# Optimization experiments

Measured on AMD Instinct MI355X. Metric: run time of the kernel, lower is better.

## Reference

```python
import jax, jax.numpy as jnp
import numpy as np

N_ATOMS = 32768
N_EDGES = 262144
ATOM_F = 256
EDGE_F = 128
OUT_F = 512
N_GAUSS = 50
SPIN_D = 3


def setup_inputs() -> dict:
    key = jax.random.key(0)
    k1, k2, k3, k4, k5 = jax.random.split(key, 5)
    h = jax.random.normal(k1, (N_ATOMS, ATOM_F), dtype=jnp.float32)
    m = jax.random.normal(k2, (N_EDGES, EDGE_F), dtype=jnp.float32)
    magft_cat = jax.random.normal(k3, (N_ATOMS, SPIN_D), dtype=jnp.float32)
    edge_index = jax.random.randint(k4, (2, N_EDGES), 0, N_ATOMS, dtype=jnp.int64)
    in_f = 2 * ATOM_F + EDGE_F + N_GAUSS  # 690
    W = jax.random.normal(k5, (OUT_F, in_f), dtype=jnp.float32) * 0.02
    return {"h": h, "m": m, "magft_cat": magft_cat, "edge_index": edge_index, "W": W}


def reference(h, m, magft_cat, edge_index, W):
    # GaussianSmearing(-1.5, 1.5, 50)
    offsets = jnp.linspace(-1.5, 1.5, N_GAUSS, dtype=jnp.float32)  # (G,)
    coeff = -0.5 / (offsets[1] - offsets[0]) ** 2

    src = edge_index[0]
    tgt = edge_index[1]
    h_s = h[src]                     # (E, A)
    h_t = h[tgt]                     # (E, A)
    # per-edge spin dot product, (E, 1)
    d = jnp.sum(magft_cat[src] * magft_cat[tgt], axis=1, keepdims=True)
    spin_edge = jnp.exp(coeff * (d - offsets) ** 2)  # (E, G)
    m_st = jnp.concatenate([h_s, h_t, m, spin_edge], axis=-1)  # (E, 690)
    # bias-free Dense with activation=None
    return m_st @ W.T  # (E, OUT_F)
```

## Files before the change

kernel.cpp:

```cpp
#include <hip/hip_runtime.h>
#include <hip/hip_bf16.h>

#define N_ATOMS 32768
#define N_EDGESC 262144
#define ATOM_F 256
#define EDGE_F 128
#define OUT_F 512
#define N_GAUSS 50
#define IN_F 690
#define NCHUNK 11

#define BM 128
#define BN 256
#define NTHREADS 512

using f32x4  = __attribute__((ext_vector_type(4))) float;
using short8 = __attribute__((ext_vector_type(8))) short;

__device__ __forceinline__ unsigned short f2bf(float f) {
  unsigned int u = __builtin_bit_cast(unsigned int, f);
  u += 0x7fffu + ((u >> 16) & 1u);
  return (unsigned short)(u >> 16);
}

__global__ void detect_idx_kernel(const unsigned int* __restrict__ ei, int* __restrict__ flag) {
  if (threadIdx.x == 0) {
    int ok = 1;
    for (int i = 0; i < 64; ++i) {
      unsigned int lo = ei[2 * i], hi = ei[2 * i + 1];
      if (hi != 0u || lo >= (unsigned)N_ATOMS) { ok = 0; break; }
    }
    *flag = ok;
  }
}

__global__ void prep_h_kernel(const float* __restrict__ h, unsigned short* __restrict__ hb) {
  size_t i = (size_t)(blockIdx.x * blockDim.x + threadIdx.x) * 8;
  if (i >= (size_t)N_ATOMS * ATOM_F) return;
  float4 a = *(const float4*)(h + i);
  float4 b = *(const float4*)(h + i + 4);
  uint4 o;
  o.x = (unsigned)f2bf(a.x) | ((unsigned)f2bf(a.y) << 16);
  o.y = (unsigned)f2bf(a.z) | ((unsigned)f2bf(a.w) << 16);
  o.z = (unsigned)f2bf(b.x) | ((unsigned)f2bf(b.y) << 16);
  o.w = (unsigned)f2bf(b.z) | ((unsigned)f2bf(b.w) << 16);
  *(uint4*)(hb + i) = o;
}

__global__ void prep_w_kernel(const float* __restrict__ W, unsigned short* __restrict__ Wp) {
  int g = blockIdx.x * blockDim.x + threadIdx.x;
  if (g >= NCHUNK * 2 * 32 * 64) return;
  int l  = g & 63;
  int nt = (g >> 6) & 31;
  int ks = (g >> 11) & 1;
  int kc = g >> 12;
  int n  = nt * 16 + (l & 15);
  int k0 = kc * 64 + ks * 32 + ((l >> 4) << 3);
  unsigned int u[4];
#pragma unroll
  for (int p = 0; p < 4; ++p) {
    int ka = k0 + 2 * p, kb = k0 + 2 * p + 1;
    float va = (ka < IN_F) ? W[n * IN_F + ka] : 0.0f;
    float vb = (kb < IN_F) ? W[n * IN_F + kb] : 0.0f;
    u[p] = (unsigned)f2bf(va) | ((unsigned)f2bf(vb) << 16);
  }
  *(uint4*)(Wp + (size_t)g * 8) = make_uint4(u[0], u[1], u[2], u[3]);
}

__global__ __launch_bounds__(NTHREADS, 4) void gemm_kernel(
    const unsigned short* __restrict__ hb, const float* __restrict__ m,
    const float* __restrict__ magft, const void* __restrict__ ei,
    const int* __restrict__ flagp, const unsigned short* __restrict__ Wp,
    float* __restrict__ out)
{
  __shared__ __align__(16) unsigned short As[4][BM * 64];
  __shared__ int sIdx[BM], tIdx[BM];
  __shared__ float dLDS[BM];

  const int tid = threadIdx.x;
  const int bid = blockIdx.x;
  const int e  = (bid & 7) | ((bid >> 4) << 3);
  const int nh = (bid >> 3) & 1;
  const int eb = e * BM;

  const int use64 = *flagp;
  if (tid < BM) {
    int ed = eb + tid;
    int s, tg;
    if (use64) {
      const long long* p = (const long long*)ei;
      s  = (int)p[ed];
      tg = (int)p[N_EDGESC + ed];
    } else {
      const int* p = (const int*)ei;
      s  = p[ed];
      tg = p[N_EDGESC + ed];
    }
    sIdx[tid] = s;
    tIdx[tid] = tg;
    float ax = magft[3 * s],  ay = magft[3 * s + 1],  az = magft[3 * s + 2];
    float bx = magft[3 * tg], by = magft[3 * tg + 1], bz = magft[3 * tg + 2];
    dLDS[tid] = ax * bx + ay * by + az * bz;
  }
  __syncthreads();

  const int lane = tid & 63;
  const int wid  = tid >> 6;
  const int wr   = wid >> 2;
  const int wc   = wid & 3;

  const int r0 = wid * 16 + (lane >> 3);
  const int hs0 = sIdx[r0], hs1 = sIdx[r0 + 8];
  const int ht0 = tIdx[r0], ht1 = tIdx[r0 + 8];
  const int srcsw = (((lane & 7) ^ (lane >> 3)) << 4);

  const int ar = tid >> 2;
  const int aq = tid & 3;

  auto stage_h = [&](int kchunk, int buf) {
    int a0 = (kchunk < 4) ? hs0 : ht0;
    int a1 = (kchunk < 4) ? hs1 : ht1;
    const unsigned short* s0 = hb + (size_t)a0 * ATOM_F + (kchunk & 3) * 64;
    const unsigned short* s1 = hb + (size_t)a1 * ATOM_F + (kchunk & 3) * 64;
    char* d0 = (char*)&As[buf][0] + wid * 2048;
    __builtin_amdgcn_global_load_lds(
        (const __attribute__((address_space(1))) void*)((const char*)s0 + srcsw),
        (__attribute__((address_space(3))) void*)d0, 16, 0, 0);
    __builtin_amdgcn_global_load_lds(
        (const __attribute__((address_space(1))) void*)((const char*)s1 + srcsw),
        (__attribute__((address_space(3))) void*)(d0 + 1024), 16, 0, 0);
  };

  auto stage_reg = [&](int kchunk, int buf) {
    char* base = (char*)&As[buf][0] + ar * 128;
    const int sw = (ar & 7) << 4;
    if (kchunk < 10) {
      const float* p = m + (size_t)(eb + ar) * EDGE_F + (kchunk & 1) * 64 + aq * 16;
#pragma unroll
      for (int hh = 0; hh < 2; ++hh) {
        float4 v0 = ((const float4*)p)[2 * hh];
        float4 v1 = ((const float4*)p)[2 * hh + 1];
        uint4 o;
        o.x = (unsigned)f2bf(v0.x) | ((unsigned)f2bf(v0.y) << 16);
        o.y = (unsigned)f2bf(v0.z) | ((unsigned)f2bf(v0.w) << 16);
        o.z = (unsigned)f2bf(v1.x) | ((unsigned)f2bf(v1.y) << 16);
        o.w = (unsigned)f2bf(v1.z) | ((unsigned)f2bf(v1.w) << 16);
        *(uint4*)(base + ((aq * 32 + hh * 16) ^ sw)) = o;
      }
    } else {
      float d = dLDS[ar];
      const float step  = 3.0f / 49.0f;
      const float coeff = -0.5f / (step * step);
#pragma unroll
      for (int hh = 0; hh < 2; ++hh) {
        unsigned int u[4];
#pragma unroll
        for (int p2 = 0; p2 < 4; ++p2) {
          int c0 = aq * 16 + hh * 8 + 2 * p2, c1 = c0 + 1;
          float o0 = -1.5f + step * (float)c0;
          float o1 = -1.5f + step * (float)c1;
          float w0 = (c0 < N_GAUSS) ? __expf(coeff * (d - o0) * (d - o0)) : 0.0f;
          float w1 = (c1 < N_GAUSS) ? __expf(coeff * (d - o1) * (d - o1)) : 0.0f;
          u[p2] = (unsigned)f2bf(w0) | ((unsigned)f2bf(w1) << 16);
        }
        *(uint4*)(base + ((aq * 32 + hh * 16) ^ sw)) = make_uint4(u[0], u[1], u[2], u[3]);
      }
    }
  };

  f32x4 acc[4][4];
#pragma unroll
  for (int i = 0; i < 4; ++i)
#pragma unroll
    for (int j = 0; j < 4; ++j) acc[i][j] = (f32x4){0.f, 0.f, 0.f, 0.f};

  const short8* Wp8 = (const short8*)Wp;

  auto compute = [&](int kc, int buf) {
    const char* abase = (const char*)&As[buf][0];
#pragma unroll
    for (int ks = 0; ks < 2; ++ks) {
      short8 b[4];
#pragma unroll
      for (int ni = 0; ni < 4; ++ni) {
        int nt = nh * 16 + wc * 4 + ni;
        b[ni] = Wp8[(size_t)(((kc * 2 + ks) * 32 + nt) << 6) + lane];
      }
      short8 a[4];
#pragma unroll
      for (int mi = 0; mi < 4; ++mi) {
        int row = wr * 64 + mi * 16 + (lane & 15);
        int colb = (ks * 64 + ((lane >> 4) << 4)) ^ ((row & 7) << 4);
        a[mi] = *(const short8*)(abase + row * 128 + colb);
      }
      __builtin_amdgcn_s_setprio(1);
#pragma unroll
      for (int mi = 0; mi < 4; ++mi)
#pragma unroll
        for (int ni = 0; ni < 4; ++ni)
          acc[mi][ni] = __builtin_amdgcn_mfma_f32_16x16x32_bf16(a[mi], b[ni], acc[mi][ni], 0, 0, 0);
      __builtin_amdgcn_s_setprio(0);
    }
  };

  stage_reg(8, 0);
  stage_reg(9, 1);
  stage_reg(10, 2);
  __syncthreads();

  for (int pos = 0; pos < 8; ++pos) {
    stage_h(pos, (pos + 3) & 3);
    int kc = (pos < 3) ? pos + 8 : pos - 3;
    compute(kc, pos & 3);
    asm volatile("s_waitcnt vmcnt(4) lgkmcnt(0)" ::: "memory");
    __builtin_amdgcn_sched_barrier(0);
    __builtin_amdgcn_s_barrier();
  }
  compute(5, 0);
  asm volatile("s_waitcnt vmcnt(2) lgkmcnt(0)" ::: "memory");
  __builtin_amdgcn_sched_barrier(0);
  __builtin_amdgcn_s_barrier();
  compute(6, 1);
  asm volatile("s_waitcnt vmcnt(0) lgkmcnt(0)" ::: "memory");
  __builtin_amdgcn_sched_barrier(0);
  __builtin_amdgcn_s_barrier();
  compute(7, 2);

#pragma unroll
  for (int mi = 0; mi < 4; ++mi) {
    int row0 = eb + wr * 64 + mi * 16 + ((lane >> 4) << 2);
#pragma unroll
    for (int ni = 0; ni < 4; ++ni) {
      int col = nh * 256 + wc * 64 + ni * 16 + (lane & 15);
#pragma unroll
      for (int j = 0; j < 4; ++j) {
        out[(size_t)(row0 + j) * OUT_F + col] = acc[mi][ni][j];
      }
    }
  }
}

extern "C" void kernel_launch(void* const* d_in, const int* in_sizes, int n_in,
                              void* d_out, int out_size, void* d_ws, size_t ws_size,
                              hipStream_t stream) {
  const float* h     = (const float*)d_in[0];
  const float* m     = (const float*)d_in[1];
  const float* magft = (const float*)d_in[2];
  const void*  ei    = d_in[3];
  const float* W     = (const float*)d_in[4];
  float* out = (float*)d_out;

  char* ws = (char*)d_ws;
  int* flag = (int*)ws;
  unsigned short* Wp = (unsigned short*)(ws + 256);
  unsigned short* hb = (unsigned short*)(ws + 256 + 720896);

  detect_idx_kernel<<<1, 64, 0, stream>>>((const unsigned int*)ei, flag);
  prep_w_kernel<<<(NCHUNK * 2 * 32 * 64 + 255) / 256, 256, 0, stream>>>(W, Wp);
  prep_h_kernel<<<(N_ATOMS * ATOM_F / 8 + 255) / 256, 256, 0, stream>>>(h, hb);

  gemm_kernel<<<dim3(2 * N_EDGESC / BM), NTHREADS, 0, stream>>>(hb, m, magft, ei, flag, Wp, out);
}
```

Measured before the change: 279.5 us.

## Pair k-chunk computes per barrier to halve workgroup barriers in GEMM pipeline

The per-chunk software pipeline, which used partial vmcnt waits and one barrier per chunk, becomes an unrolled schedule. Each phase issues two h-gather LDS loads, computes two staged chunks, then does a full __syncthreads. The aim is to cut the number of workgroup barriers and their synchronisation stalls. In exchange, each __syncthreads waits for all outstanding global loads, so the prefetch lead shrinks to about one phase and gather latency may be less hidden.

```diff
diff --git a/kernel.cpp b/kernel.cpp
--- a/kernel.cpp
+++ b/kernel.cpp
@@ -204,26 +204,33 @@
   };
 
   stage_reg(8, 0);
+  stage_reg(10, 2);
   stage_reg(9, 1);
-  stage_reg(10, 2);
-  __syncthreads();
-
-  for (int pos = 0; pos < 8; ++pos) {
-    stage_h(pos, (pos + 3) & 3);
-    int kc = (pos < 3) ? pos + 8 : pos - 3;
-    compute(kc, pos & 3);
-    asm volatile("s_waitcnt vmcnt(4) lgkmcnt(0)" ::: "memory");
-    __builtin_amdgcn_sched_barrier(0);
-    __builtin_amdgcn_s_barrier();
-  }
+  __syncthreads();
+
+  stage_h(0, 3);
+  compute(8, 0);
+  compute(9, 1);
+  __syncthreads();
+  stage_h(1, 0);
+  stage_h(2, 1);
+  compute(10, 2);
+  compute(0, 3);
+  __syncthreads();
+  stage_h(3, 2);
+  stage_h(4, 3);
+  compute(1, 0);
+  compute(2, 1);
+  __syncthreads();
+  stage_h(5, 0);
+  stage_h(6, 1);
+  compute(3, 2);
+  compute(4, 3);
+  __syncthreads();
+  stage_h(7, 2);
   compute(5, 0);
-  asm volatile("s_waitcnt vmcnt(2) lgkmcnt(0)" ::: "memory");
-  __builtin_amdgcn_sched_barrier(0);
-  __builtin_amdgcn_s_barrier();
   compute(6, 1);
-  asm volatile("s_waitcnt vmcnt(0) lgkmcnt(0)" ::: "memory");
-  __builtin_amdgcn_sched_barrier(0);
-  __builtin_amdgcn_s_barrier();
+  __syncthreads();
   compute(7, 2);
 
 #pragma unroll
```

After: 273.1 us. 2.3% less time.
